# Kernel optimization log

Hardware: AMD Instinct MI355X
Metric: run time of the kernel (lower is better)

## Reference

```python
import jax, jax.numpy as jnp
import numpy as np

N = 8192      # total factor-graph rows (detection nodes + association nodes)
ND = N // 2   # detection-node rows; rest are association (edge) rows
D_RAW = 74    # raw input dim; last 10 cols = convex hull (5 points x 2 coords)
EPS = 1e-5    # BatchNorm eps


def _adjs():
    # signed factor-graph adjacencies with self-loops marking row type
    rng = np.random.RandomState(0)
    deg = 8
    node_adj = np.zeros((N, N), np.float32)
    edge_adj = np.zeros((N, N), np.float32)
    nbr = rng.randint(ND, N, size=(ND, deg))
    node_adj[np.repeat(np.arange(ND), deg), nbr.ravel()] = rng.choice([-1.0, 1.0], ND * deg).astype(np.float32)
    node_adj[np.arange(ND), np.arange(ND)] = 1.0
    nbr2 = rng.randint(0, ND, size=(N - ND, deg))
    edge_adj[np.repeat(np.arange(ND, N), deg), nbr2.ravel()] = rng.choice([-1.0, 1.0], (N - ND) * deg).astype(np.float32)
    edge_adj[np.arange(ND, N), np.arange(ND, N)] = 1.0
    return jnp.asarray(node_adj), jnp.asarray(edge_adj)


def setup_inputs() -> dict:
    key = jax.random.key(0)
    ks = jax.random.split(key, 16)
    node_adj, edge_adj = _adjs()

    def lin(k, fi, fo):
        return jax.random.normal(k, (fi, fo), jnp.float32) / np.sqrt(fi)

    inp = {"x": jax.random.normal(ks[0], (N, D_RAW), jnp.float32),
           "node_adj": node_adj, "edge_adj": edge_adj}
    # PointNetfeatsmall: 1x1 conv stack 3->16->32->64 with eval-mode BatchNorm
    for i, (fi, fo) in enumerate([(3, 16), (16, 32), (32, 64)], 1):
        k = jax.random.split(ks[i], 5)
        inp[f"pn_w{i}"] = lin(k[0], fi, fo)
        inp[f"pn_b{i}"] = 0.1 * jax.random.normal(k[1], (fo,), jnp.float32)
        inp[f"pn_g{i}"] = 1.0 + 0.1 * jax.random.normal(k[2], (fo,), jnp.float32)
        inp[f"pn_be{i}"] = 0.1 * jax.random.normal(k[3], (fo,), jnp.float32)
        inp[f"pn_m{i}"] = 0.1 * jax.random.normal(k[4], (fo,), jnp.float32)
        inp[f"pn_v{i}"] = jnp.ones((fo,), jnp.float32)
    # FactorGraphConvolution weights (msg_type='concat' -> in dim doubles)
    for i, (fi, fo) in enumerate([(256, 64), (128, 64), (128, 1)], 1):
        k = jax.random.split(ks[10 + i], 2)
        inp[f"gc{i}_wn"] = lin(k[0], fi, fo)
        inp[f"gc{i}_we"] = lin(k[1], fi, fo)
        inp[f"gc{i}_bn"] = jnp.zeros((fo,), jnp.float32)
        inp[f"gc{i}_be"] = jnp.zeros((fo,), jnp.float32)
    inp["gc3_bn"] = jnp.full((1,), -4.595, jnp.float32)  # nn.init.constant_ in TrackMPNN.__init__
    inp["gc3_be"] = jnp.full((1,), 4.595, jnp.float32)
    return inp


def _bn(h, g, b, m, v):  # h: [N, C, P], eval-mode BatchNorm1d
    return (h - m[:, None]) * (g[:, None] / jnp.sqrt(v[:, None] + EPS)) + b[:, None]


def _fgc(h, node_adj, edge_adj, wn, we, bn_, be_, relu):
    # concat(self, aggregated-neighbors) -> linear; node/edge rows use their own branch
    node_out = jnp.concatenate([h, node_adj @ h], axis=1) @ wn + bn_
    edge_out = jnp.concatenate([h, edge_adj @ h], axis=1) @ we + be_
    out = jnp.where((jnp.diag(node_adj) != 0)[:, None], node_out, edge_out)
    return jax.nn.relu(out) if relu else out


def reference(x, node_adj, edge_adj,
              pn_w1, pn_b1, pn_g1, pn_be1, pn_m1, pn_v1,
              pn_w2, pn_b2, pn_g2, pn_be2, pn_m2, pn_v2,
              pn_w3, pn_b3, pn_g3, pn_be3, pn_m3, pn_v3,
              gc1_wn, gc1_we, gc1_bn, gc1_be,
              gc2_wn, gc2_we, gc2_bn, gc2_be,
              gc3_wn, gc3_we, gc3_bn, gc3_be):
    # convex hull branch: [N, 3, 5] (third coordinate zero-padded)
    ch = jnp.concatenate([x[:, -10:].reshape(-1, 2, 5),
                          jnp.zeros((x.shape[0], 1, 5), x.dtype)], axis=1)
    h = jax.nn.relu(_bn(jnp.einsum('ncp,cd->ndp', ch, pn_w1) + pn_b1[:, None], pn_g1, pn_be1, pn_m1, pn_v1))
    h = jax.nn.relu(_bn(jnp.einsum('ncp,cd->ndp', h, pn_w2) + pn_b2[:, None], pn_g2, pn_be2, pn_m2, pn_v2))
    h = _bn(jnp.einsum('ncp,cd->ndp', h, pn_w3) + pn_b3[:, None], pn_g3, pn_be3, pn_m3, pn_v3)
    feat = h.max(axis=2)                       # PointNet global max pool -> [N, 64]
    h = jnp.concatenate([x[:, :-10], feat], axis=1)  # [N, 128]
    h = _fgc(h, node_adj, edge_adj, gc1_wn, gc1_we, gc1_bn, gc1_be, True)
    h = _fgc(h, node_adj, edge_adj, gc2_wn, gc2_we, gc2_bn, gc2_be, True)
    h = _fgc(h, node_adj, edge_adj, gc3_wn, gc3_we, gc3_bn, gc3_be, False)
    return jax.nn.sigmoid(h)                   # [N, 1]
```

## Files before the change

### kernel.cpp

```cpp
#include <hip/hip_runtime.h>
#include <math.h>

#define NROWS 8192
#define NDET  4096

static constexpr int OFF_SGN = 65536;
static constexpr int OFF_PN  = 131072;
static constexpr int OFF_AGG = 655360;
static constexpr int OFF_H1  = 1703936;
static constexpr int OFF_H2  = 2228224;

__global__ __launch_bounds__(256) void k_extract(
    const float* __restrict__ nodeA, const float* __restrict__ edgeA,
    int* __restrict__ idx, float* __restrict__ sgn)
{
    int row = blockIdx.x, t = threadIdx.x;
    const float* src; int col0;
    if (row < NDET) { src = nodeA + (size_t)row * NROWS + NDET; col0 = NDET; }
    else            { src = edgeA + (size_t)row * NROWS;        col0 = 0;    }
    __shared__ int scnt;
    if (t == 0) scnt = 0;
    __syncthreads();
    const float4* s4 = (const float4*)src;
    #pragma unroll
    for (int it = 0; it < 4; ++it) {
        float4 v = s4[t + it * 256];
        int cb = col0 + (t + it * 256) * 4;
        if (v.x != 0.f) { int p = atomicAdd(&scnt, 1); idx[row * 8 + p] = cb;     sgn[row * 8 + p] = v.x; }
        if (v.y != 0.f) { int p = atomicAdd(&scnt, 1); idx[row * 8 + p] = cb + 1; sgn[row * 8 + p] = v.y; }
        if (v.z != 0.f) { int p = atomicAdd(&scnt, 1); idx[row * 8 + p] = cb + 2; sgn[row * 8 + p] = v.z; }
        if (v.w != 0.f) { int p = atomicAdd(&scnt, 1); idx[row * 8 + p] = cb + 3; sgn[row * 8 + p] = v.w; }
    }
    __syncthreads();
    for (int p = scnt + t; p < 8; p += 256) { idx[row * 8 + p] = 0; sgn[row * 8 + p] = 0.f; }
}

__global__ __launch_bounds__(256) void k_pointnet(
    const float* __restrict__ x,
    const float* __restrict__ w1, const float* __restrict__ b1,
    const float* __restrict__ g1, const float* __restrict__ be1,
    const float* __restrict__ m1, const float* __restrict__ v1,
    const float* __restrict__ w2, const float* __restrict__ b2,
    const float* __restrict__ g2, const float* __restrict__ be2,
    const float* __restrict__ m2, const float* __restrict__ v2,
    const float* __restrict__ w3, const float* __restrict__ b3,
    const float* __restrict__ g3, const float* __restrict__ be3,
    const float* __restrict__ m3, const float* __restrict__ v3,
    float* __restrict__ pn)
{
    __shared__ float fw[2720];
    int t = threadIdx.x;
    for (int i = t; i < 48; i += 256)  { int d = i & 15; fw[i]       = w1[i] * g1[d] * rsqrtf(v1[d] + 1e-5f); }
    for (int i = t; i < 16; i += 256)  {                 fw[48 + i]  = (b1[i] - m1[i]) * g1[i] * rsqrtf(v1[i] + 1e-5f) + be1[i]; }
    for (int i = t; i < 512; i += 256) { int d = i & 31; fw[64 + i]  = w2[i] * g2[d] * rsqrtf(v2[d] + 1e-5f); }
    for (int i = t; i < 32; i += 256)  {                 fw[576 + i] = (b2[i] - m2[i]) * g2[i] * rsqrtf(v2[i] + 1e-5f) + be2[i]; }
    for (int i = t; i < 2048; i += 256){ int d = i & 63; fw[608 + i] = w3[i] * g3[d] * rsqrtf(v3[d] + 1e-5f); }
    for (int i = t; i < 64; i += 256)  {                 fw[2656 + i]= (b3[i] - m3[i]) * g3[i] * rsqrtf(v3[i] + 1e-5f) + be3[i]; }
    __syncthreads();

    int lane = t & 63;
    int wv   = t >> 6;
    int l15  = lane & 15, l31 = lane & 31;
    int rowbase = (blockIdx.x * 4 + wv) * 4;

    for (int r = rowbase; r < rowbase + 4; ++r) {
        float val  = (lane < 10) ? x[(size_t)r * 74 + 64 + lane] : 0.f;
        float vmax = -3.0e38f;
        #pragma unroll
        for (int p = 0; p < 5; ++p) {
            float a0 = __shfl(val, p, 64);
            float a1 = __shfl(val, p + 5, 64);
            float h1v = fmaxf(0.f, a0 * fw[l15] + a1 * fw[16 + l15] + fw[48 + l15]);
            float s2 = fw[576 + l31];
            #pragma unroll
            for (int d = 0; d < 16; ++d)
                s2 += __shfl(h1v, d, 64) * fw[64 + d * 32 + l31];
            float h2v = fmaxf(0.f, s2);
            float s3 = fw[2656 + lane];
            #pragma unroll
            for (int e = 0; e < 32; ++e)
                s3 += __shfl(h2v, e, 64) * fw[608 + e * 64 + lane];
            vmax = fmaxf(vmax, s3);
        }
        pn[(size_t)r * 64 + lane] = vmax;
    }
}

__global__ __launch_bounds__(256) void k_gather1(
    const float* __restrict__ x, const float* __restrict__ pn,
    const int* __restrict__ idx, const float* __restrict__ sgn,
    float* __restrict__ agg)
{
    int lane = threadIdx.x & 63;
    int row  = blockIdx.x * 4 + (threadIdx.x >> 6);
    float acc0 = x[(size_t)row * 74 + lane];
    float acc1 = pn[(size_t)row * 64 + lane];
    #pragma unroll
    for (int j = 0; j < 8; ++j) {
        int nb   = idx[row * 8 + j];
        float sg = sgn[row * 8 + j];
        acc0 += sg * x[(size_t)nb * 74 + lane];
        acc1 += sg * pn[(size_t)nb * 64 + lane];
    }
    agg[(size_t)row * 128 + lane]      = acc0;
    agg[(size_t)row * 128 + 64 + lane] = acc1;
}

__global__ __launch_bounds__(256) void k_gather2(
    const float* __restrict__ h, const int* __restrict__ idx,
    const float* __restrict__ sgn, float* __restrict__ agg)
{
    int lane = threadIdx.x & 63;
    int row  = blockIdx.x * 4 + (threadIdx.x >> 6);
    float acc = h[(size_t)row * 64 + lane];
    #pragma unroll
    for (int j = 0; j < 8; ++j) {
        int nb   = idx[row * 8 + j];
        float sg = sgn[row * 8 + j];
        acc += sg * h[(size_t)nb * 64 + lane];
    }
    agg[(size_t)row * 64 + lane] = acc;
}

__global__ __launch_bounds__(256) void k_gemm1(
    const float* __restrict__ x, const float* __restrict__ pn,
    const float* __restrict__ agg,
    const float* __restrict__ wn, const float* __restrict__ we,
    const float* __restrict__ bn, const float* __restrict__ be,
    float* __restrict__ out)
{
    int r_l = threadIdx.x >> 2, cg = threadIdx.x & 3;
    int row = blockIdx.x * 64 + r_l;
    int c0  = blockIdx.y * 16 + cg * 4;
    bool isnode = blockIdx.x < 64;
    const float* W = isnode ? wn : we;
    const float* B = isnode ? bn : be;
    float acc[4] = {B[c0], B[c0 + 1], B[c0 + 2], B[c0 + 3]};

    const float2* x2 = (const float2*)(x + (size_t)row * 74);
    #pragma unroll
    for (int kg = 0; kg < 32; ++kg) {
        float2 v = x2[kg];
        float4 wv0 = *(const float4*)&W[(kg * 2) * 64 + c0];
        float4 wv1 = *(const float4*)&W[(kg * 2 + 1) * 64 + c0];
        acc[0] += v.x * wv0.x + v.y * wv1.x;
        acc[1] += v.x * wv0.y + v.y * wv1.y;
        acc[2] += v.x * wv0.z + v.y * wv1.z;
        acc[3] += v.x * wv0.w + v.y * wv1.w;
    }
    const float4* p4 = (const float4*)(pn + (size_t)row * 64);
    #pragma unroll
    for (int kg = 0; kg < 16; ++kg) {
        float4 v = p4[kg];
        const float* vv = &v.x;
        #pragma unroll
        for (int kk = 0; kk < 4; ++kk) {
            float4 wv = *(const float4*)&W[(64 + kg * 4 + kk) * 64 + c0];
            acc[0] += vv[kk] * wv.x; acc[1] += vv[kk] * wv.y;
            acc[2] += vv[kk] * wv.z; acc[3] += vv[kk] * wv.w;
        }
    }
    const float4* a4 = (const float4*)(agg + (size_t)row * 128);
    #pragma unroll
    for (int kg = 0; kg < 32; ++kg) {
        float4 v = a4[kg];
        const float* vv = &v.x;
        #pragma unroll
        for (int kk = 0; kk < 4; ++kk) {
            float4 wv = *(const float4*)&W[(128 + kg * 4 + kk) * 64 + c0];
            acc[0] += vv[kk] * wv.x; acc[1] += vv[kk] * wv.y;
            acc[2] += vv[kk] * wv.z; acc[3] += vv[kk] * wv.w;
        }
    }
    float4 o;
    o.x = fmaxf(acc[0], 0.f); o.y = fmaxf(acc[1], 0.f);
    o.z = fmaxf(acc[2], 0.f); o.w = fmaxf(acc[3], 0.f);
    *(float4*)&out[(size_t)row * 64 + c0] = o;
}

__global__ __launch_bounds__(256) void k_gemm2(
    const float* __restrict__ h, const float* __restrict__ agg,
    const float* __restrict__ wn, const float* __restrict__ we,
    const float* __restrict__ bn, const float* __restrict__ be,
    float* __restrict__ out)
{
    int r_l = threadIdx.x >> 2, cg = threadIdx.x & 3;
    int row = blockIdx.x * 64 + r_l;
    int c0  = blockIdx.y * 16 + cg * 4;
    bool isnode = blockIdx.x < 64;
    const float* W = isnode ? wn : we;
    const float* B = isnode ? bn : be;
    float acc[4] = {B[c0], B[c0 + 1], B[c0 + 2], B[c0 + 3]};

    const float4* h4 = (const float4*)(h + (size_t)row * 64);
    const float4* a4 = (const float4*)(agg + (size_t)row * 64);
    #pragma unroll
    for (int kg = 0; kg < 16; ++kg) {
        float4 v = h4[kg];
        const float* vv = &v.x;
        #pragma unroll
        for (int kk = 0; kk < 4; ++kk) {
            float4 wv = *(const float4*)&W[(kg * 4 + kk) * 64 + c0];
            acc[0] += vv[kk] * wv.x; acc[1] += vv[kk] * wv.y;
            acc[2] += vv[kk] * wv.z; acc[3] += vv[kk] * wv.w;
        }
    }
    #pragma unroll
    for (int kg = 0; kg < 16; ++kg) {
        float4 v = a4[kg];
        const float* vv = &v.x;
        #pragma unroll
        for (int kk = 0; kk < 4; ++kk) {
            float4 wv = *(const float4*)&W[(64 + kg * 4 + kk) * 64 + c0];
            acc[0] += vv[kk] * wv.x; acc[1] += vv[kk] * wv.y;
            acc[2] += vv[kk] * wv.z; acc[3] += vv[kk] * wv.w;
        }
    }
    float4 o;
    o.x = fmaxf(acc[0], 0.f); o.y = fmaxf(acc[1], 0.f);
    o.z = fmaxf(acc[2], 0.f); o.w = fmaxf(acc[3], 0.f);
    *(float4*)&out[(size_t)row * 64 + c0] = o;
}

__global__ __launch_bounds__(256) void k_gc3(
    const float* __restrict__ h2, const int* __restrict__ idx,
    const float* __restrict__ sgn,
    const float* __restrict__ wn, const float* __restrict__ we,
    const float* __restrict__ bn, const float* __restrict__ be,
    float* __restrict__ out)
{
    int lane = threadIdx.x & 63;
    int row  = blockIdx.x * 4 + (threadIdx.x >> 6);
    float own = h2[(size_t)row * 64 + lane];
    float agg = own;
    #pragma unroll
    for (int j = 0; j < 8; ++j) {
        int nb   = idx[row * 8 + j];
        float sg = sgn[row * 8 + j];
        agg += sg * h2[(size_t)nb * 64 + lane];
    }
    bool isnode = row < NDET;
    const float* w = isnode ? wn : we;
    float bias = isnode ? bn[0] : be[0];
    float acc = own * w[lane] + agg * w[64 + lane];
    #pragma unroll
    for (int off = 32; off > 0; off >>= 1)
        acc += __shfl_xor(acc, off, 64);
    if (lane == 0)
        out[row] = 1.f / (1.f + expf(-(acc + bias)));
}

extern "C" void kernel_launch(void* const* d_in, const int* in_sizes, int n_in,
                              void* d_out, int out_size, void* d_ws, size_t ws_size,
                              hipStream_t stream)
{
    const float* x     = (const float*)d_in[0];
    const float* nodeA = (const float*)d_in[1];
    const float* edgeA = (const float*)d_in[2];
    const float* pw1 = (const float*)d_in[3];  const float* pb1 = (const float*)d_in[4];
    const float* pg1 = (const float*)d_in[5];  const float* pe1 = (const float*)d_in[6];
    const float* pm1 = (const float*)d_in[7];  const float* pv1 = (const float*)d_in[8];
    const float* pw2 = (const float*)d_in[9];  const float* pb2 = (const float*)d_in[10];
    const float* pg2 = (const float*)d_in[11]; const float* pe2 = (const float*)d_in[12];
    const float* pm2 = (const float*)d_in[13]; const float* pv2 = (const float*)d_in[14];
    const float* pw3 = (const float*)d_in[15]; const float* pb3 = (const float*)d_in[16];
    const float* pg3 = (const float*)d_in[17]; const float* pe3 = (const float*)d_in[18];
    const float* pm3 = (const float*)d_in[19]; const float* pv3 = (const float*)d_in[20];
    const float* g1wn = (const float*)d_in[21]; const float* g1we = (const float*)d_in[22];
    const float* g1bn = (const float*)d_in[23]; const float* g1be = (const float*)d_in[24];
    const float* g2wn = (const float*)d_in[25]; const float* g2we = (const float*)d_in[26];
    const float* g2bn = (const float*)d_in[27]; const float* g2be = (const float*)d_in[28];
    const float* g3wn = (const float*)d_in[29]; const float* g3we = (const float*)d_in[30];
    const float* g3bn = (const float*)d_in[31]; const float* g3be = (const float*)d_in[32];

    float* ws  = (float*)d_ws;
    int*   idx = (int*)ws;
    float* sgn = ws + OFF_SGN;
    float* pn  = ws + OFF_PN;
    float* agg = ws + OFF_AGG;
    float* h1  = ws + OFF_H1;
    float* h2  = ws + OFF_H2;
    float* out = (float*)d_out;

    k_extract<<<NROWS, 256, 0, stream>>>(nodeA, edgeA, idx, sgn);
    k_pointnet<<<512, 256, 0, stream>>>(x,
        pw1, pb1, pg1, pe1, pm1, pv1,
        pw2, pb2, pg2, pe2, pm2, pv2,
        pw3, pb3, pg3, pe3, pm3, pv3, pn);
    k_gather1<<<2048, 256, 0, stream>>>(x, pn, idx, sgn, agg);
    k_gemm1<<<dim3(128, 4), 256, 0, stream>>>(x, pn, agg, g1wn, g1we, g1bn, g1be, h1);
    k_gather2<<<2048, 256, 0, stream>>>(h1, idx, sgn, agg);
    k_gemm2<<<dim3(128, 4), 256, 0, stream>>>(h1, agg, g2wn, g2we, g2bn, g2be, h2);
    k_gc3<<<2048, 256, 0, stream>>>(h2, idx, sgn, g3wn, g3we, g3bn, g3be, out);
}
```

Measured before the change: 550.6 us.

## Fuse neighbor gather with dense GEMM for first two graph conv layers

Merges the separate gather and GEMM kernels of layers 1 and 2 into one kernel per layer. Each block gathers signed neighbor sums for 16 rows into shared memory and multiplies them by the weights there. This removes the global aggregation buffer write and read, and two kernel launches. The cost is fewer blocks (512) and each block now computing all 64 output columns.

```diff
diff --git a/kernel.cpp b/kernel.cpp
--- a/kernel.cpp
+++ b/kernel.cpp
@@ -6,7 +6,6 @@
 
 static constexpr int OFF_SGN = 65536;
 static constexpr int OFF_PN  = 131072;
-static constexpr int OFF_AGG = 655360;
 static constexpr int OFF_H1  = 1703936;
 static constexpr int OFF_H2  = 2228224;
 
@@ -86,140 +85,125 @@
     }
 }
 
-__global__ __launch_bounds__(256) void k_gather1(
+__global__ __launch_bounds__(256) void k_fgc1(
     const float* __restrict__ x, const float* __restrict__ pn,
     const int* __restrict__ idx, const float* __restrict__ sgn,
-    float* __restrict__ agg)
-{
-    int lane = threadIdx.x & 63;
-    int row  = blockIdx.x * 4 + (threadIdx.x >> 6);
-    float acc0 = x[(size_t)row * 74 + lane];
-    float acc1 = pn[(size_t)row * 64 + lane];
-    #pragma unroll
-    for (int j = 0; j < 8; ++j) {
-        int nb   = idx[row * 8 + j];
-        float sg = sgn[row * 8 + j];
-        acc0 += sg * x[(size_t)nb * 74 + lane];
-        acc1 += sg * pn[(size_t)nb * 64 + lane];
-    }
-    agg[(size_t)row * 128 + lane]      = acc0;
-    agg[(size_t)row * 128 + 64 + lane] = acc1;
-}
-
-__global__ __launch_bounds__(256) void k_gather2(
-    const float* __restrict__ h, const int* __restrict__ idx,
-    const float* __restrict__ sgn, float* __restrict__ agg)
-{
-    int lane = threadIdx.x & 63;
-    int row  = blockIdx.x * 4 + (threadIdx.x >> 6);
-    float acc = h[(size_t)row * 64 + lane];
-    #pragma unroll
-    for (int j = 0; j < 8; ++j) {
-        int nb   = idx[row * 8 + j];
-        float sg = sgn[row * 8 + j];
-        acc += sg * h[(size_t)nb * 64 + lane];
-    }
-    agg[(size_t)row * 64 + lane] = acc;
-}
-
-__global__ __launch_bounds__(256) void k_gemm1(
-    const float* __restrict__ x, const float* __restrict__ pn,
-    const float* __restrict__ agg,
     const float* __restrict__ wn, const float* __restrict__ we,
     const float* __restrict__ bn, const float* __restrict__ be,
     float* __restrict__ out)
 {
-    int r_l = threadIdx.x >> 2, cg = threadIdx.x & 3;
-    int row = blockIdx.x * 64 + r_l;
-    int c0  = blockIdx.y * 16 + cg * 4;
-    bool isnode = blockIdx.x < 64;
+    __shared__ float inb[16 * 260];
+    __shared__ int   lidx[128];
+    __shared__ float lsgn[128];
+    int t = threadIdx.x;
+    int r0 = blockIdx.x * 16;
+    if (t < 128) {
+        int ir = t >> 3, j = t & 7;
+        lidx[t] = idx[(r0 + ir) * 8 + j];
+        lsgn[t] = sgn[(r0 + ir) * 8 + j];
+    }
+    __syncthreads();
+
+    int f   = t & 127;
+    int rrb = t >> 7;
+    #pragma unroll
+    for (int pass = 0; pass < 8; ++pass) {
+        int rr = rrb + pass * 2;
+        int r  = r0 + rr;
+        float own = (f < 64) ? x[(size_t)r * 74 + f] : pn[(size_t)r * 64 + (f - 64)];
+        float acc = own;
+        #pragma unroll
+        for (int j = 0; j < 8; ++j) {
+            int nb   = lidx[rr * 8 + j];
+            float sg = lsgn[rr * 8 + j];
+            float v  = (f < 64) ? x[(size_t)nb * 74 + f] : pn[(size_t)nb * 64 + (f - 64)];
+            acc += sg * v;
+        }
+        inb[rr * 260 + f]       = own;
+        inb[rr * 260 + 128 + f] = acc;
+    }
+    __syncthreads();
+
+    int r_l = t >> 4, cg = t & 15, c0 = cg * 4;
+    bool isnode = (blockIdx.x < 256);
     const float* W = isnode ? wn : we;
     const float* B = isnode ? bn : be;
-    float acc[4] = {B[c0], B[c0 + 1], B[c0 + 2], B[c0 + 3]};
-
-    const float2* x2 = (const float2*)(x + (size_t)row * 74);
-    #pragma unroll
-    for (int kg = 0; kg < 32; ++kg) {
-        float2 v = x2[kg];
-        float4 wv0 = *(const float4*)&W[(kg * 2) * 64 + c0];
-        float4 wv1 = *(const float4*)&W[(kg * 2 + 1) * 64 + c0];
-        acc[0] += v.x * wv0.x + v.y * wv1.x;
-        acc[1] += v.x * wv0.y + v.y * wv1.y;
-        acc[2] += v.x * wv0.z + v.y * wv1.z;
-        acc[3] += v.x * wv0.w + v.y * wv1.w;
-    }
-    const float4* p4 = (const float4*)(pn + (size_t)row * 64);
-    #pragma unroll
-    for (int kg = 0; kg < 16; ++kg) {
-        float4 v = p4[kg];
-        const float* vv = &v.x;
+    float a0 = B[c0], a1 = B[c0 + 1], a2 = B[c0 + 2], a3 = B[c0 + 3];
+    #pragma unroll
+    for (int kg = 0; kg < 64; ++kg) {
+        float4 a = *(const float4*)&inb[r_l * 260 + kg * 4];
+        const float* av = &a.x;
         #pragma unroll
         for (int kk = 0; kk < 4; ++kk) {
-            float4 wv = *(const float4*)&W[(64 + kg * 4 + kk) * 64 + c0];
-            acc[0] += vv[kk] * wv.x; acc[1] += vv[kk] * wv.y;
-            acc[2] += vv[kk] * wv.z; acc[3] += vv[kk] * wv.w;
-        }
-    }
-    const float4* a4 = (const float4*)(agg + (size_t)row * 128);
-    #pragma unroll
-    for (int kg = 0; kg < 32; ++kg) {
-        float4 v = a4[kg];
-        const float* vv = &v.x;
-        #pragma unroll
-        for (int kk = 0; kk < 4; ++kk) {
-            float4 wv = *(const float4*)&W[(128 + kg * 4 + kk) * 64 + c0];
-            acc[0] += vv[kk] * wv.x; acc[1] += vv[kk] * wv.y;
-            acc[2] += vv[kk] * wv.z; acc[3] += vv[kk] * wv.w;
+            float4 w = *(const float4*)&W[(kg * 4 + kk) * 64 + c0];
+            a0 += av[kk] * w.x; a1 += av[kk] * w.y;
+            a2 += av[kk] * w.z; a3 += av[kk] * w.w;
         }
     }
     float4 o;
-    o.x = fmaxf(acc[0], 0.f); o.y = fmaxf(acc[1], 0.f);
-    o.z = fmaxf(acc[2], 0.f); o.w = fmaxf(acc[3], 0.f);
-    *(float4*)&out[(size_t)row * 64 + c0] = o;
-}
-
-__global__ __launch_bounds__(256) void k_gemm2(
-    const float* __restrict__ h, const float* __restrict__ agg,
+    o.x = fmaxf(a0, 0.f); o.y = fmaxf(a1, 0.f);
+    o.z = fmaxf(a2, 0.f); o.w = fmaxf(a3, 0.f);
+    *(float4*)&out[(size_t)(r0 + r_l) * 64 + c0] = o;
+}
+
+__global__ __launch_bounds__(256) void k_fgc2(
+    const float* __restrict__ h, const int* __restrict__ idx,
+    const float* __restrict__ sgn,
     const float* __restrict__ wn, const float* __restrict__ we,
     const float* __restrict__ bn, const float* __restrict__ be,
     float* __restrict__ out)
 {
-    int r_l = threadIdx.x >> 2, cg = threadIdx.x & 3;
-    int row = blockIdx.x * 64 + r_l;
-    int c0  = blockIdx.y * 16 + cg * 4;
-    bool isnode = blockIdx.x < 64;
+    __shared__ float inb[16 * 132];
+    __shared__ int   lidx[128];
+    __shared__ float lsgn[128];
+    int t = threadIdx.x;
+    int r0 = blockIdx.x * 16;
+    if (t < 128) {
+        int ir = t >> 3, j = t & 7;
+        lidx[t] = idx[(r0 + ir) * 8 + j];
+        lsgn[t] = sgn[(r0 + ir) * 8 + j];
+    }
+    __syncthreads();
+
+    int f   = t & 63;
+    int rrb = t >> 6;
+    #pragma unroll
+    for (int pass = 0; pass < 4; ++pass) {
+        int rr = rrb + pass * 4;
+        int r  = r0 + rr;
+        float own = h[(size_t)r * 64 + f];
+        float acc = own;
+        #pragma unroll
+        for (int j = 0; j < 8; ++j) {
+            int nb   = lidx[rr * 8 + j];
+            float sg = lsgn[rr * 8 + j];
+            acc += sg * h[(size_t)nb * 64 + f];
+        }
+        inb[rr * 132 + f]      = own;
+        inb[rr * 132 + 64 + f] = acc;
+    }
+    __syncthreads();
+
+    int r_l = t >> 4, cg = t & 15, c0 = cg * 4;
+    bool isnode = (blockIdx.x < 256);
     const float* W = isnode ? wn : we;
     const float* B = isnode ? bn : be;
-    float acc[4] = {B[c0], B[c0 + 1], B[c0 + 2], B[c0 + 3]};
-
-    const float4* h4 = (const float4*)(h + (size_t)row * 64);
-    const float4* a4 = (const float4*)(agg + (size_t)row * 64);
-    #pragma unroll
-    for (int kg = 0; kg < 16; ++kg) {
-        float4 v = h4[kg];
-        const float* vv = &v.x;
+    float a0 = B[c0], a1 = B[c0 + 1], a2 = B[c0 + 2], a3 = B[c0 + 3];
+    #pragma unroll
+    for (int kg = 0; kg < 32; ++kg) {
+        float4 a = *(const float4*)&inb[r_l * 132 + kg * 4];
+        const float* av = &a.x;
         #pragma unroll
         for (int kk = 0; kk < 4; ++kk) {
-            float4 wv = *(const float4*)&W[(kg * 4 + kk) * 64 + c0];
-            acc[0] += vv[kk] * wv.x; acc[1] += vv[kk] * wv.y;
-            acc[2] += vv[kk] * wv.z; acc[3] += vv[kk] * wv.w;
-        }
-    }
-    #pragma unroll
-    for (int kg = 0; kg < 16; ++kg) {
-        float4 v = a4[kg];
-        const float* vv = &v.x;
-        #pragma unroll
-        for (int kk = 0; kk < 4; ++kk) {
-            float4 wv = *(const float4*)&W[(64 + kg * 4 + kk) * 64 + c0];
-            acc[0] += vv[kk] * wv.x; acc[1] += vv[kk] * wv.y;
-            acc[2] += vv[kk] * wv.z; acc[3] += vv[kk] * wv.w;
+            float4 w = *(const float4*)&W[(kg * 4 + kk) * 64 + c0];
+            a0 += av[kk] * w.x; a1 += av[kk] * w.y;
+            a2 += av[kk] * w.z; a3 += av[kk] * w.w;
         }
     }
     float4 o;
-    o.x = fmaxf(acc[0], 0.f); o.y = fmaxf(acc[1], 0.f);
-    o.z = fmaxf(acc[2], 0.f); o.w = fmaxf(acc[3], 0.f);
-    *(float4*)&out[(size_t)row * 64 + c0] = o;
+    o.x = fmaxf(a0, 0.f); o.y = fmaxf(a1, 0.f);
+    o.z = fmaxf(a2, 0.f); o.w = fmaxf(a3, 0.f);
+    *(float4*)&out[(size_t)(r0 + r_l) * 64 + c0] = o;
 }
 
 __global__ __launch_bounds__(256) void k_gc3(
@@ -277,7 +261,6 @@
     int*   idx = (int*)ws;
     float* sgn = ws + OFF_SGN;
     float* pn  = ws + OFF_PN;
-    float* agg = ws + OFF_AGG;
     float* h1  = ws + OFF_H1;
     float* h2  = ws + OFF_H2;
     float* out = (float*)d_out;
@@ -287,9 +270,7 @@
         pw1, pb1, pg1, pe1, pm1, pv1,
         pw2, pb2, pg2, pe2, pm2, pv2,
         pw3, pb3, pg3, pe3, pm3, pv3, pn);
-    k_gather1<<<2048, 256, 0, stream>>>(x, pn, idx, sgn, agg);
-    k_gemm1<<<dim3(128, 4), 256, 0, stream>>>(x, pn, agg, g1wn, g1we, g1bn, g1be, h1);
-    k_gather2<<<2048, 256, 0, stream>>>(h1, idx, sgn, agg);
-    k_gemm2<<<dim3(128, 4), 256, 0, stream>>>(h1, agg, g2wn, g2we, g2bn, g2be, h2);
+    k_fgc1<<<512, 256, 0, stream>>>(x, pn, idx, sgn, g1wn, g1we, g1bn, g1be, h1);
+    k_fgc2<<<512, 256, 0, stream>>>(h1, idx, sgn, g2wn, g2we, g2bn, g2be, h2);
     k_gc3<<<2048, 256, 0, stream>>>(h2, idx, sgn, g3wn, g3we, g3bn, g3be, out);
 }
```

After: 545.0 us. Within noise of the previous version (-1.0%).
